# Kernel tuning notes

Hardware: AMD Instinct MI355X
Metric: run time of the kernel (lower is better)

## Reference

```python
import jax, jax.numpy as jnp
import numpy as np

ALPHA = 1.702
LIMIT = 7.0
TOP_K = 2


def setup_inputs() -> dict:
    key = jax.random.key(0)
    ks = jax.random.split(key, 5)
    B, S, H, M, E = 2, 512, 1024, 4096, 16
    glorot = jax.nn.initializers.glorot_uniform()
    return {
        "hidden_states": jax.random.normal(ks[0], (B, S, H), dtype=jnp.float32),
        "router_w": glorot(ks[1], (H, E), jnp.float32),
        "router_b": jnp.zeros((E,), jnp.float32),
        "gate_up_proj": glorot(ks[2], (E, H, 2 * M), jnp.float32),
        "gate_up_proj_bias": jnp.zeros((E, 2 * M), jnp.float32),
        "down_proj": glorot(ks[3], (E, M, H), jnp.float32),
        "down_proj_bias": jnp.zeros((E, H), jnp.float32),
    }


def _moe_forward(x, router_w, router_b, gate_up_proj, gate_up_proj_bias,
                 down_proj, down_proj_bias):
    B, S, H = x.shape
    E = router_w.shape[1]
    xt = x.reshape(-1, H)  # [T, H]
    T = xt.shape[0]

    # --- Router: top-k logits -> softmax over selected -> dense [T, E] scores ---
    logits = xt @ router_w + router_b                       # [T, E]
    top_vals, top_idx = jax.lax.top_k(logits, TOP_K)        # [T, K]
    top_w = jax.nn.softmax(top_vals, axis=-1)               # [T, K]
    router_scores = jnp.zeros((T, E), dtype=top_w.dtype).at[
        jnp.arange(T)[:, None], top_idx].add(top_w)         # [T, E]

    # --- Dense all-expert GLU-FFN (GPT-OSS dense MoE trick) ---
    gate_up = jnp.einsum('th,ehm->etm', xt, gate_up_proj)   # [E, T, 2M]
    gate_up = gate_up + gate_up_proj_bias[:, None, :]
    gate = gate_up[..., ::2]                                # interleaved split
    up = gate_up[..., 1::2]
    gate = jnp.clip(gate, -1e9, LIMIT)
    up = jnp.clip(up, -LIMIT, LIMIT)
    glu = gate * jax.nn.sigmoid(gate * ALPHA)
    gated = (up + 1.0) * glu                                # [E, T, M]
    out = jnp.einsum('etm,emh->eth', gated, down_proj)
    out = out + down_proj_bias[:, None, :]                  # [E, T, H]

    # --- Weighted combine over experts ---
    final = jnp.einsum('eth,te->th', out, router_scores)    # [T, H]
    return final.reshape(B, S, H), router_scores


def reference(hidden_states, router_w, router_b, gate_up_proj,
              gate_up_proj_bias, down_proj, down_proj_bias):
    return _moe_forward(hidden_states, router_w, router_b, gate_up_proj,
                        gate_up_proj_bias, down_proj, down_proj_bias)
```

## Files before the change

### kernel.cpp

```cpp
#include <hip/hip_runtime.h>
#include <hip/hip_bf16.h>
#include <cstdint>
#include <cstddef>

typedef unsigned short u16;
typedef __bf16 v8bf __attribute__((ext_vector_type(8)));
typedef float v4f __attribute__((ext_vector_type(4)));

#define T_TOK 1024
#define H_DIM 1024
#define E_NUM 16
#define M_DIM 4096
#define GU_DIM 8192
#define ALPHA 1.702f
#define LIMIT 7.0f
#define LDSTR 40
#define KSPL 4

#define WS_COUNTS   0
#define WS_OFFSETS  256
#define WS_TOKE     512
#define WS_TOKP     (WS_TOKE + 8192)
#define WS_TOKW     (WS_TOKP + 8192)
#define WS_TOKG     (WS_TOKW + 8192)
#define WS_SLOTTOK  (WS_TOKG + 8192)
#define WS_XG       65536
#define WS_GATED    (WS_XG + 2048*1024*2)
#define WS_OUT      (WS_GATED + (size_t)2048*4096*2)

static __device__ __forceinline__ u16 f2bf(float f) {
    union { __hip_bfloat16 b; u16 u; } cv;
    cv.b = __float2bfloat16(f);
    return cv.u;
}

__global__ __launch_bounds__(64) void k_zero(int* counts) {
    if (threadIdx.x < E_NUM) counts[threadIdx.x] = 0;
}

__global__ __launch_bounds__(64) void k_router(
    const float* __restrict__ x, const float* __restrict__ rw, const float* __restrict__ rb,
    float* __restrict__ scores, int* __restrict__ counts,
    int* __restrict__ tok_e, int* __restrict__ tok_p, float* __restrict__ tok_w)
{
    const int t = blockIdx.x;
    const int lane = threadIdx.x;
    float part[E_NUM];
#pragma unroll
    for (int e = 0; e < E_NUM; ++e) part[e] = 0.f;
    const float* xrow = x + (size_t)t * H_DIM;
    for (int h = lane; h < H_DIM; h += 64) {
        float xv = xrow[h];
        const float* wrow = rw + (size_t)h * E_NUM;
#pragma unroll
        for (int e = 0; e < E_NUM; ++e) part[e] = fmaf(xv, wrow[e], part[e]);
    }
    __shared__ float red[64][E_NUM];
    __shared__ float logits[E_NUM];
    __shared__ int se[2];
    __shared__ float sw[2];
#pragma unroll
    for (int e = 0; e < E_NUM; ++e) red[lane][e] = part[e];
    __syncthreads();
    if (lane < E_NUM) {
        float s = rb[lane];
        for (int l = 0; l < 64; ++l) s += red[l][lane];
        logits[lane] = s;
    }
    __syncthreads();
    if (lane == 0) {
        int i0 = 0; float v0 = logits[0];
        for (int e = 1; e < E_NUM; ++e) { float v = logits[e]; if (v > v0) { v0 = v; i0 = e; } }
        int i1 = -1; float v1 = -3.4e38f;
        for (int e = 0; e < E_NUM; ++e) {
            if (e == i0) continue;
            float v = logits[e];
            if (v > v1) { v1 = v; i1 = e; }
        }
        float ex = expf(v1 - v0);
        float w0 = 1.f / (1.f + ex);
        float w1 = ex / (1.f + ex);
        int p0 = atomicAdd(&counts[i0], 1);
        int p1 = atomicAdd(&counts[i1], 1);
        tok_e[2*t]   = i0; tok_p[2*t]   = p0; tok_w[2*t]   = w0;
        tok_e[2*t+1] = i1; tok_p[2*t+1] = p1; tok_w[2*t+1] = w1;
        se[0] = i0; se[1] = i1; sw[0] = w0; sw[1] = w1;
    }
    __syncthreads();
    if (lane < E_NUM) {
        float v = 0.f;
        if (lane == se[0]) v = sw[0];
        else if (lane == se[1]) v = sw[1];
        scores[(size_t)t * E_NUM + lane] = v;
    }
}

__global__ __launch_bounds__(64) void k_offsets(const int* __restrict__ counts, int* __restrict__ offsets) {
    if (threadIdx.x == 0) {
        int acc = 0;
        for (int e = 0; e < E_NUM; ++e) { offsets[e] = acc; acc += counts[e]; }
        offsets[E_NUM] = acc;
    }
}

__global__ __launch_bounds__(256) void k_build(
    const int* __restrict__ tok_e, const int* __restrict__ tok_p, const int* __restrict__ offsets,
    int* __restrict__ tok_g, int* __restrict__ slot_tok)
{
    int i = blockIdx.x * blockDim.x + threadIdx.x;
    if (i >= 2 * T_TOK) return;
    int e = tok_e[i], p = tok_p[i];
    int g = offsets[e] + p;
    tok_g[i] = g;
    slot_tok[g] = i >> 1;
}

__global__ __launch_bounds__(256) void k_gather(
    const float* __restrict__ x, const int* __restrict__ slot_tok, u16* __restrict__ xg)
{
    const int g = blockIdx.x;
    const int t = slot_tok[g];
    const float4* src = (const float4*)(x + (size_t)t * H_DIM);
    float4 v = src[threadIdx.x];
    ushort4 o;
    o.x = f2bf(v.x); o.y = f2bf(v.y); o.z = f2bf(v.z); o.w = f2bf(v.w);
    *(ushort4*)&xg[(size_t)g * H_DIM + threadIdx.x * 4] = o;
}

__global__ __launch_bounds__(512) void k_gateup(
    const u16* __restrict__ xg, const float* __restrict__ W, const float* __restrict__ bias,
    const int* __restrict__ counts, const int* __restrict__ offsets,
    u16* __restrict__ gated)
{
    const int e = blockIdx.z;
    const int cnt = counts[e];
    const int row0 = blockIdx.y * 256;
    if (row0 >= cnt) return;
    const int m0 = blockIdx.x * 64;
    const int off = offsets[e];
    __shared__ u16 As[256 * LDSTR];
    __shared__ u16 Bs[128 * LDSTR];
    const int tid = threadIdx.x;
    const int lane = tid & 63;
    const int w = tid >> 6;
    const bool active = (row0 + w * 32) < cnt;

    const int ar0 = tid >> 2, aseg = tid & 3;
    const int ar1 = ar0 + 128;
    int gr0 = row0 + ar0; if (gr0 >= cnt) gr0 = cnt - 1;
    int gr1 = row0 + ar1; if (gr1 >= cnt) gr1 = cnt - 1;
    const u16* aP0 = xg + (size_t)(off + gr0) * H_DIM + aseg * 8;
    const u16* aP1 = xg + (size_t)(off + gr1) * H_DIM + aseg * 8;

    const int bn   = tid & 127;
    const int bk0  = (tid >> 7) * 8;
    const int bcol = (bn >> 1) + (bn & 1) * 64;
    const float* bP = W + (size_t)e * H_DIM * GU_DIM + (size_t)bk0 * GU_DIM + 2 * m0 + bn;

    uint4 ra0, ra1;
    float rbA[8], rbB[8];
    v4f acc0[8], acc1[8];
    v4f zz = {0.f, 0.f, 0.f, 0.f};
#pragma unroll
    for (int f = 0; f < 8; ++f) { acc0[f] = zz; acc1[f] = zz; }

    const u16* aF = &As[(w * 32 + (lane & 15)) * LDSTR + (lane >> 4) * 8];
    const u16* bF = &Bs[(lane & 15) * LDSTR + (lane >> 4) * 8];

#define GU_LOADA(K0)                                                      \
    ra0 = *(const uint4*)(aP0 + (K0));                                    \
    ra1 = *(const uint4*)(aP1 + (K0));

#define GU_LOADB(K0, dst)                                                 \
    _Pragma("unroll")                                                     \
    for (int i = 0; i < 8; ++i) dst[i] = bP[(size_t)((K0) + i) * GU_DIM];

#define GU_STORE(rbX)                                                     \
    *(uint4*)&As[ar0 * LDSTR + aseg * 8] = ra0;                           \
    *(uint4*)&As[ar1 * LDSTR + aseg * 8] = ra1;                           \
    {                                                                     \
        uint4 p0;                                                         \
        p0.x = f2bf(rbX[0]) | ((unsigned)f2bf(rbX[1]) << 16);             \
        p0.y = f2bf(rbX[2]) | ((unsigned)f2bf(rbX[3]) << 16);             \
        p0.z = f2bf(rbX[4]) | ((unsigned)f2bf(rbX[5]) << 16);             \
        p0.w = f2bf(rbX[6]) | ((unsigned)f2bf(rbX[7]) << 16);             \
        *(uint4*)&Bs[bcol * LDSTR + bk0] = p0;                            \
    }

#define GU_MFMA                                                           \
    if (active) {                                                         \
        v8bf a0 = *(const v8bf*)aF;                                       \
        v8bf a1 = *(const v8bf*)(aF + 16 * LDSTR);                        \
        _Pragma("unroll")                                                 \
        for (int f = 0; f < 8; ++f) {                                     \
            v8bf b = *(const v8bf*)(bF + f * 16 * LDSTR);                 \
            acc0[f] = __builtin_amdgcn_mfma_f32_16x16x32_bf16(a0, b, acc0[f], 0, 0, 0); \
            acc1[f] = __builtin_amdgcn_mfma_f32_16x16x32_bf16(a1, b, acc1[f], 0, 0, 0); \
        }                                                                 \
    }

    GU_LOADA(0)
    GU_LOADB(0, rbA)
    GU_LOADB(32, rbB)
    for (int k0 = 0; k0 < H_DIM; k0 += 64) {
        GU_STORE(rbA)
        __syncthreads();
        GU_LOADA(k0 + 32)
        if (k0 + 64 < H_DIM) { GU_LOADB(k0 + 64, rbA) }
        GU_MFMA
        __syncthreads();
        GU_STORE(rbB)
        __syncthreads();
        if (k0 + 64 < H_DIM) { GU_LOADA(k0 + 64) }
        if (k0 + 96 < H_DIM) { GU_LOADB(k0 + 96, rbB) }
        GU_MFMA
        __syncthreads();
    }
#undef GU_LOADA
#undef GU_LOADB
#undef GU_STORE
#undef GU_MFMA

    if (!active) return;
    const float* bg = bias + (size_t)e * GU_DIM + 2 * m0;
#pragma unroll
    for (int i = 0; i < 2; ++i) {
#pragma unroll
        for (int r = 0; r < 4; ++r) {
            int rr = row0 + w * 32 + i * 16 + (lane >> 4) * 4 + r;
            if (rr >= cnt) continue;
            u16* orow = gated + (size_t)(off + rr) * M_DIM + m0;
#pragma unroll
            for (int f = 0; f < 4; ++f) {
                int ml = f * 16 + (lane & 15);
                float g = (i ? acc1[f][r]     : acc0[f][r])     + bg[2 * ml];
                float u = (i ? acc1[f + 4][r] : acc0[f + 4][r]) + bg[2 * ml + 1];
                g = fminf(g, LIMIT); g = fmaxf(g, -1e9f);
                u = fminf(fmaxf(u, -LIMIT), LIMIT);
                float glu = g / (1.f + expf(-ALPHA * g));
                orow[ml] = f2bf((u + 1.f) * glu);
            }
        }
    }
}

__global__ __launch_bounds__(512) void k_down(
    const u16* __restrict__ gated, const float* __restrict__ W,
    const int* __restrict__ counts, const int* __restrict__ offsets,
    float* __restrict__ outws)
{
    const int e = blockIdx.z;
    const int cnt = counts[e];
    const int row0 = blockIdx.y * 256;
    if (row0 >= cnt) return;
    const int ntile = blockIdx.x & 15;
    const int kc = blockIdx.x >> 4;
    const int c0 = ntile * 64;
    const int kbase = kc * (M_DIM / KSPL);
    const int off = offsets[e];
    __shared__ u16 As[256 * LDSTR];
    __shared__ u16 Bs[64 * LDSTR];
    const int tid = threadIdx.x;
    const int lane = tid & 63;
    const int w = tid >> 6;
    const bool active = (row0 + w * 32) < cnt;

    const int ar0 = tid >> 2, aseg = tid & 3;
    const int ar1 = ar0 + 128;
    int gr0 = row0 + ar0; if (gr0 >= cnt) gr0 = cnt - 1;
    int gr1 = row0 + ar1; if (gr1 >= cnt) gr1 = cnt - 1;
    const u16* aP0 = gated + (size_t)(off + gr0) * M_DIM + kbase + aseg * 8;
    const u16* aP1 = gated + (size_t)(off + gr1) * M_DIM + kbase + aseg * 8;

    const int bn  = tid & 63;
    const int bk0 = (tid >> 6) * 4;
    const float* bP = W + (size_t)e * M_DIM * H_DIM + (size_t)(kbase + bk0) * H_DIM + c0 + bn;

    uint4 ra0, ra1;
    float rbA[4], rbB[4];
    v4f acc0[4], acc1[4];
    v4f zz = {0.f, 0.f, 0.f, 0.f};
#pragma unroll
    for (int f = 0; f < 4; ++f) { acc0[f] = zz; acc1[f] = zz; }

    const u16* aF = &As[(w * 32 + (lane & 15)) * LDSTR + (lane >> 4) * 8];
    const u16* bF = &Bs[(lane & 15) * LDSTR + (lane >> 4) * 8];

#define DN_LOADA(K0)                                                      \
    ra0 = *(const uint4*)(aP0 + (K0));                                    \
    ra1 = *(const uint4*)(aP1 + (K0));

#define DN_LOADB(K0, dst)                                                 \
    _Pragma("unroll")                                                     \
    for (int i = 0; i < 4; ++i) dst[i] = bP[(size_t)((K0) + i) * H_DIM];

#define DN_STORE(rbX)                                                     \
    *(uint4*)&As[ar0 * LDSTR + aseg * 8] = ra0;                           \
    *(uint4*)&As[ar1 * LDSTR + aseg * 8] = ra1;                           \
    {                                                                     \
        uint2 p0;                                                         \
        p0.x = f2bf(rbX[0]) | ((unsigned)f2bf(rbX[1]) << 16);             \
        p0.y = f2bf(rbX[2]) | ((unsigned)f2bf(rbX[3]) << 16);             \
        *(uint2*)&Bs[bn * LDSTR + bk0] = p0;                              \
    }

#define DN_MFMA                                                           \
    if (active) {                                                         \
        v8bf a0 = *(const v8bf*)aF;                                       \
        v8bf a1 = *(const v8bf*)(aF + 16 * LDSTR);                        \
        _Pragma("unroll")                                                 \
        for (int f = 0; f < 4; ++f) {                                     \
            v8bf b = *(const v8bf*)(bF + f * 16 * LDSTR);                 \
            acc0[f] = __builtin_amdgcn_mfma_f32_16x16x32_bf16(a0, b, acc0[f], 0, 0, 0); \
            acc1[f] = __builtin_amdgcn_mfma_f32_16x16x32_bf16(a1, b, acc1[f], 0, 0, 0); \
        }                                                                 \
    }

    const int KC = M_DIM / KSPL;
    DN_LOADA(0)
    DN_LOADB(0, rbA)
    DN_LOADB(32, rbB)
    for (int k0 = 0; k0 < KC; k0 += 64) {
        DN_STORE(rbA)
        __syncthreads();
        DN_LOADA(k0 + 32)
        if (k0 + 64 < KC) { DN_LOADB(k0 + 64, rbA) }
        DN_MFMA
        __syncthreads();
        DN_STORE(rbB)
        __syncthreads();
        if (k0 + 64 < KC) { DN_LOADA(k0 + 64) }
        if (k0 + 96 < KC) { DN_LOADB(k0 + 96, rbB) }
        DN_MFMA
        __syncthreads();
    }
#undef DN_LOADA
#undef DN_LOADB
#undef DN_STORE
#undef DN_MFMA

    if (!active) return;
    float* outp = outws + (size_t)kc * 2048 * H_DIM;
#pragma unroll
    for (int i = 0; i < 2; ++i) {
#pragma unroll
        for (int r = 0; r < 4; ++r) {
            int rr = row0 + w * 32 + i * 16 + (lane >> 4) * 4 + r;
            if (rr >= cnt) continue;
            float* orow = outp + (size_t)(off + rr) * H_DIM + c0;
#pragma unroll
            for (int f = 0; f < 4; ++f) {
                orow[f * 16 + (lane & 15)] = (i ? acc1[f][r] : acc0[f][r]);
            }
        }
    }
}

__global__ __launch_bounds__(256) void k_final(
    const float* __restrict__ outws, const float* __restrict__ db,
    const int* __restrict__ tok_e, const int* __restrict__ tok_g, const float* __restrict__ tok_w,
    float* __restrict__ out)
{
    const int t = blockIdx.x;
    const int tid = threadIdx.x;
    const int h = tid << 2;
    const int e0 = tok_e[2*t], e1 = tok_e[2*t+1];
    const int g0 = tok_g[2*t], g1 = tok_g[2*t+1];
    const float w0 = tok_w[2*t], w1 = tok_w[2*t+1];
    float4 o0 = {0,0,0,0}, o1 = {0,0,0,0};
#pragma unroll
    for (int p = 0; p < KSPL; ++p) {
        const float* base = outws + (size_t)p * 2048 * H_DIM;
        float4 a = *(const float4*)(base + (size_t)g0 * H_DIM + h);
        float4 b = *(const float4*)(base + (size_t)g1 * H_DIM + h);
        o0.x += a.x; o0.y += a.y; o0.z += a.z; o0.w += a.w;
        o1.x += b.x; o1.y += b.y; o1.z += b.z; o1.w += b.w;
    }
    float4 b0 = *(const float4*)(db + (size_t)e0 * H_DIM + h);
    float4 b1 = *(const float4*)(db + (size_t)e1 * H_DIM + h);
    float4 r;
    r.x = w0 * (o0.x + b0.x) + w1 * (o1.x + b1.x);
    r.y = w0 * (o0.y + b0.y) + w1 * (o1.y + b1.y);
    r.z = w0 * (o0.z + b0.z) + w1 * (o1.z + b1.z);
    r.w = w0 * (o0.w + b0.w) + w1 * (o1.w + b1.w);
    *(float4*)(out + (size_t)t * H_DIM + h) = r;
}

extern "C" void kernel_launch(void* const* d_in, const int* in_sizes, int n_in,
                              void* d_out, int out_size, void* d_ws, size_t ws_size,
                              hipStream_t stream) {
    const float* x     = (const float*)d_in[0];
    const float* rw    = (const float*)d_in[1];
    const float* rb    = (const float*)d_in[2];
    const float* gup   = (const float*)d_in[3];
    const float* gup_b = (const float*)d_in[4];
    const float* dw    = (const float*)d_in[5];
    const float* db    = (const float*)d_in[6];
    float* out    = (float*)d_out;
    float* scores = out + (size_t)T_TOK * H_DIM;

    char* ws = (char*)d_ws;
    int*   counts   = (int*)(ws + WS_COUNTS);
    int*   offsets  = (int*)(ws + WS_OFFSETS);
    int*   tok_e    = (int*)(ws + WS_TOKE);
    int*   tok_p    = (int*)(ws + WS_TOKP);
    float* tok_w    = (float*)(ws + WS_TOKW);
    int*   tok_g    = (int*)(ws + WS_TOKG);
    int*   slot_tok = (int*)(ws + WS_SLOTTOK);
    u16*   xg       = (u16*)(ws + WS_XG);
    u16*   gated    = (u16*)(ws + WS_GATED);
    float* outws    = (float*)(ws + WS_OUT);

    k_zero<<<1, 64, 0, stream>>>(counts);
    k_router<<<T_TOK, 64, 0, stream>>>(x, rw, rb, scores, counts, tok_e, tok_p, tok_w);
    k_offsets<<<1, 64, 0, stream>>>(counts, offsets);
    k_build<<<(2*T_TOK + 255)/256, 256, 0, stream>>>(tok_e, tok_p, offsets, tok_g, slot_tok);
    k_gather<<<2*T_TOK, 256, 0, stream>>>(x, slot_tok, xg);
    dim3 g2(M_DIM/64, 8, E_NUM);
    k_gateup<<<g2, 512, 0, stream>>>(xg, gup, gup_b, counts, offsets, gated);
    dim3 g3(16 * KSPL, 8, E_NUM);
    k_down<<<g3, 512, 0, stream>>>(gated, dw, counts, offsets, outws);
    k_final<<<T_TOK, 256, 0, stream>>>(outws, db, tok_e, tok_g, tok_w, out);
}
```

Baseline: 270.1 us.

## Double-buffer LDS with deeper prefetch in expert GEMMs and fuse routing kernels

The gate-up and down GEMMs now use two LDS buffers with a four-deep register prefetch of weights, so each k-step needs one barrier instead of two. Weight loads become float2 vector loads with a rearranged LDS placement. launch_bounds gains a minimum of 4 blocks, and the offsets, build and gather kernels are merged into one scatter kernel that computes prefix offsets inline, saving two launches. The cost is more LDS and registers per block, and the occupancy hint can force register spills.

```diff
diff --git a/kernel.cpp b/kernel.cpp
--- a/kernel.cpp
+++ b/kernel.cpp
@@ -18,12 +18,10 @@
 #define KSPL 4
 
 #define WS_COUNTS   0
-#define WS_OFFSETS  256
 #define WS_TOKE     512
 #define WS_TOKP     (WS_TOKE + 8192)
 #define WS_TOKW     (WS_TOKP + 8192)
 #define WS_TOKG     (WS_TOKW + 8192)
-#define WS_SLOTTOK  (WS_TOKG + 8192)
 #define WS_XG       65536
 #define WS_GATED    (WS_XG + 2048*1024*2)
 #define WS_OUT      (WS_GATED + (size_t)2048*4096*2)
@@ -95,51 +93,37 @@
     }
 }
 
-__global__ __launch_bounds__(64) void k_offsets(const int* __restrict__ counts, int* __restrict__ offsets) {
-    if (threadIdx.x == 0) {
-        int acc = 0;
-        for (int e = 0; e < E_NUM; ++e) { offsets[e] = acc; acc += counts[e]; }
-        offsets[E_NUM] = acc;
-    }
-}
-
-__global__ __launch_bounds__(256) void k_build(
-    const int* __restrict__ tok_e, const int* __restrict__ tok_p, const int* __restrict__ offsets,
-    int* __restrict__ tok_g, int* __restrict__ slot_tok)
+__global__ __launch_bounds__(256) void k_scatter(
+    const float* __restrict__ x, const int* __restrict__ counts,
+    const int* __restrict__ tok_e, const int* __restrict__ tok_p,
+    int* __restrict__ tok_g, u16* __restrict__ xg)
 {
-    int i = blockIdx.x * blockDim.x + threadIdx.x;
-    if (i >= 2 * T_TOK) return;
-    int e = tok_e[i], p = tok_p[i];
-    int g = offsets[e] + p;
-    tok_g[i] = g;
-    slot_tok[g] = i >> 1;
-}
-
-__global__ __launch_bounds__(256) void k_gather(
-    const float* __restrict__ x, const int* __restrict__ slot_tok, u16* __restrict__ xg)
-{
-    const int g = blockIdx.x;
-    const int t = slot_tok[g];
-    const float4* src = (const float4*)(x + (size_t)t * H_DIM);
-    float4 v = src[threadIdx.x];
+    const int i = blockIdx.x;
+    const int e = tok_e[i], p = tok_p[i];
+    int off = 0;
+#pragma unroll
+    for (int j = 0; j < E_NUM; ++j) off += (j < e) ? counts[j] : 0;
+    const int g = off + p;
+    if (threadIdx.x == 0) tok_g[i] = g;
+    const float4 v = ((const float4*)(x + (size_t)(i >> 1) * H_DIM))[threadIdx.x];
     ushort4 o;
     o.x = f2bf(v.x); o.y = f2bf(v.y); o.z = f2bf(v.z); o.w = f2bf(v.w);
     *(ushort4*)&xg[(size_t)g * H_DIM + threadIdx.x * 4] = o;
 }
 
-__global__ __launch_bounds__(512) void k_gateup(
+__global__ __launch_bounds__(512, 4) void k_gateup(
     const u16* __restrict__ xg, const float* __restrict__ W, const float* __restrict__ bias,
-    const int* __restrict__ counts, const int* __restrict__ offsets,
-    u16* __restrict__ gated)
+    const int* __restrict__ counts, u16* __restrict__ gated)
 {
     const int e = blockIdx.z;
-    const int cnt = counts[e];
+    int cnt = 0, off = 0;
+#pragma unroll
+    for (int j = 0; j < E_NUM; ++j) { int c = counts[j]; off += (j < e) ? c : 0; if (j == e) cnt = c; }
     const int row0 = blockIdx.y * 256;
     if (row0 >= cnt) return;
     const int m0 = blockIdx.x * 64;
-    const int off = offsets[e];
-    __shared__ u16 As[256 * LDSTR];
-    __shared__ u16 Bs[128 * LDSTR];
+    __shared__ u16 As[2][256 * LDSTR];
+    __shared__ u16 Bs[2][128 * LDSTR];
     const int tid = threadIdx.x;
     const int lane = tid & 63;
     const int w = tid >> 6;
@@ -152,74 +136,95 @@
     const u16* aP0 = xg + (size_t)(off + gr0) * H_DIM + aseg * 8;
     const u16* aP1 = xg + (size_t)(off + gr1) * H_DIM + aseg * 8;
 
-    const int bn   = tid & 127;
-    const int bk0  = (tid >> 7) * 8;
-    const int bcol = (bn >> 1) + (bn & 1) * 64;
-    const float* bP = W + (size_t)e * H_DIM * GU_DIM + (size_t)bk0 * GU_DIM + 2 * m0 + bn;
+    const int bc  = tid & 63;
+    const int bkg = tid >> 6;
+    const float* bP = W + (size_t)e * H_DIM * GU_DIM + (size_t)bkg * 4 * GU_DIM + 2 * m0 + 2 * bc;
 
     uint4 ra0, ra1;
-    float rbA[8], rbB[8];
+    float rb0[8], rb1[8], rb2[8], rb3[8];
     v4f acc0[8], acc1[8];
     v4f zz = {0.f, 0.f, 0.f, 0.f};
 #pragma unroll
     for (int f = 0; f < 8; ++f) { acc0[f] = zz; acc1[f] = zz; }
 
-    const u16* aF = &As[(w * 32 + (lane & 15)) * LDSTR + (lane >> 4) * 8];
-    const u16* bF = &Bs[(lane & 15) * LDSTR + (lane >> 4) * 8];
-
-#define GU_LOADA(K0)                                                      \
-    ra0 = *(const uint4*)(aP0 + (K0));                                    \
-    ra1 = *(const uint4*)(aP1 + (K0));
-
-#define GU_LOADB(K0, dst)                                                 \
-    _Pragma("unroll")                                                     \
-    for (int i = 0; i < 8; ++i) dst[i] = bP[(size_t)((K0) + i) * GU_DIM];
-
-#define GU_STORE(rbX)                                                     \
-    *(uint4*)&As[ar0 * LDSTR + aseg * 8] = ra0;                           \
-    *(uint4*)&As[ar1 * LDSTR + aseg * 8] = ra1;                           \
+    const int aFo = (w * 32 + (lane & 15)) * LDSTR + (lane >> 4) * 8;
+    const int bFo = (lane & 15) * LDSTR + (lane >> 4) * 8;
+    const int asl0 = ar0 * LDSTR + aseg * 8;
+    const int asl1 = ar1 * LDSTR + aseg * 8;
+    const int bslg = bc * LDSTR + bkg * 4;
+    const int bslu = (bc + 64) * LDSTR + bkg * 4;
+
+#define GU_LOADA(KK)                                                      \
+    ra0 = *(const uint4*)(aP0 + (KK));                                    \
+    ra1 = *(const uint4*)(aP1 + (KK));
+
+#define GU_LOADB(KK, dst)                                                 \
     {                                                                     \
-        uint4 p0;                                                         \
-        p0.x = f2bf(rbX[0]) | ((unsigned)f2bf(rbX[1]) << 16);             \
-        p0.y = f2bf(rbX[2]) | ((unsigned)f2bf(rbX[3]) << 16);             \
-        p0.z = f2bf(rbX[4]) | ((unsigned)f2bf(rbX[5]) << 16);             \
-        p0.w = f2bf(rbX[6]) | ((unsigned)f2bf(rbX[7]) << 16);             \
-        *(uint4*)&Bs[bcol * LDSTR + bk0] = p0;                            \
-    }
-
-#define GU_MFMA                                                           \
+        const float* p_ = bP + (size_t)(KK) * GU_DIM;                     \
+        float2 t0_ = *(const float2*)(p_);                                \
+        float2 t1_ = *(const float2*)(p_ + GU_DIM);                       \
+        float2 t2_ = *(const float2*)(p_ + 2 * GU_DIM);                   \
+        float2 t3_ = *(const float2*)(p_ + 3 * GU_DIM);                   \
+        dst[0]=t0_.x; dst[1]=t0_.y; dst[2]=t1_.x; dst[3]=t1_.y;           \
+        dst[4]=t2_.x; dst[5]=t2_.y; dst[6]=t3_.x; dst[7]=t3_.y;           \
+    }
+
+#define GU_STORE(BUF, rbX)                                                \
+    *(uint4*)&As[BUF][asl0] = ra0;                                        \
+    *(uint4*)&As[BUF][asl1] = ra1;                                        \
+    {                                                                     \
+        uint2 pg_, pu_;                                                   \
+        pg_.x = f2bf(rbX[0]) | ((unsigned)f2bf(rbX[2]) << 16);            \
+        pg_.y = f2bf(rbX[4]) | ((unsigned)f2bf(rbX[6]) << 16);            \
+        pu_.x = f2bf(rbX[1]) | ((unsigned)f2bf(rbX[3]) << 16);            \
+        pu_.y = f2bf(rbX[5]) | ((unsigned)f2bf(rbX[7]) << 16);            \
+        *(uint2*)&Bs[BUF][bslg] = pg_;                                    \
+        *(uint2*)&Bs[BUF][bslu] = pu_;                                    \
+    }
+
+#define GU_MFMA(BUF)                                                      \
     if (active) {                                                         \
-        v8bf a0 = *(const v8bf*)aF;                                       \
-        v8bf a1 = *(const v8bf*)(aF + 16 * LDSTR);                        \
+        v8bf a0 = *(const v8bf*)&As[BUF][aFo];                            \
+        v8bf a1 = *(const v8bf*)&As[BUF][aFo + 16 * LDSTR];               \
         _Pragma("unroll")                                                 \
         for (int f = 0; f < 8; ++f) {                                     \
-            v8bf b = *(const v8bf*)(bF + f * 16 * LDSTR);                 \
+            v8bf b = *(const v8bf*)&Bs[BUF][bFo + f * 16 * LDSTR];        \
             acc0[f] = __builtin_amdgcn_mfma_f32_16x16x32_bf16(a0, b, acc0[f], 0, 0, 0); \
             acc1[f] = __builtin_amdgcn_mfma_f32_16x16x32_bf16(a1, b, acc1[f], 0, 0, 0); \
         }                                                                 \
     }
 
     GU_LOADA(0)
-    GU_LOADB(0, rbA)
-    GU_LOADB(32, rbB)
-    for (int k0 = 0; k0 < H_DIM; k0 += 64) {
-        GU_STORE(rbA)
-        __syncthreads();
-        GU_LOADA(k0 + 32)
-        if (k0 + 64 < H_DIM) { GU_LOADB(k0 + 64, rbA) }
-        GU_MFMA
-        __syncthreads();
-        GU_STORE(rbB)
-        __syncthreads();
-        if (k0 + 64 < H_DIM) { GU_LOADA(k0 + 64) }
-        if (k0 + 96 < H_DIM) { GU_LOADB(k0 + 96, rbB) }
-        GU_MFMA
-        __syncthreads();
-    }
+    GU_LOADB(0, rb0)
+    GU_STORE(0, rb0)
+    GU_LOADA(32)
+    GU_LOADB(32, rb1)
+    GU_LOADB(64, rb2)
+    GU_LOADB(96, rb3)
+    __syncthreads();
+
+#define GU_PH(P, RBS, RBL)                                                \
+    GU_STORE((P + 1) & 1, RBS)                                            \
+    GU_LOADA((t4 + P + 2) * 32)                                           \
+    GU_LOADB((t4 + P + 4) * 32, RBL)                                      \
+    GU_MFMA(P & 1)                                                        \
+    __syncthreads();
+
+    for (int t4 = 0; t4 < 28; t4 += 4) {
+        GU_PH(0, rb1, rb0)
+        GU_PH(1, rb2, rb1)
+        GU_PH(2, rb3, rb2)
+        GU_PH(3, rb0, rb3)
+    }
+    GU_STORE(1, rb1) GU_LOADA(960) GU_MFMA(0) __syncthreads();
+    GU_STORE(0, rb2) GU_LOADA(992) GU_MFMA(1) __syncthreads();
+    GU_STORE(1, rb3) GU_MFMA(0) __syncthreads();
+    GU_MFMA(1)
 #undef GU_LOADA
 #undef GU_LOADB
 #undef GU_STORE
 #undef GU_MFMA
+#undef GU_PH
 
     if (!active) return;
     const float* bg = bias + (size_t)e * GU_DIM + 2 * m0;
@@ -244,22 +249,22 @@
     }
 }
 
-__global__ __launch_bounds__(512) void k_down(
+__global__ __launch_bounds__(512, 4) void k_down(
     const u16* __restrict__ gated, const float* __restrict__ W,
-    const int* __restrict__ counts, const int* __restrict__ offsets,
-    float* __restrict__ outws)
+    const int* __restrict__ counts, float* __restrict__ outws)
 {
     const int e = blockIdx.z;
-    const int cnt = counts[e];
+    int cnt = 0, off = 0;
+#pragma unroll
+    for (int j = 0; j < E_NUM; ++j) { int c = counts[j]; off += (j < e) ? c : 0; if (j == e) cnt = c; }
     const int row0 = blockIdx.y * 256;
     if (row0 >= cnt) return;
     const int ntile = blockIdx.x & 15;
     const int kc = blockIdx.x >> 4;
     const int c0 = ntile * 64;
     const int kbase = kc * (M_DIM / KSPL);
-    const int off = offsets[e];
-    __shared__ u16 As[256 * LDSTR];
-    __shared__ u16 Bs[64 * LDSTR];
+    __shared__ u16 As[2][256 * LDSTR];
+    __shared__ u16 Bs[2][64 * LDSTR];
     const int tid = threadIdx.x;
     const int lane = tid & 63;
     const int w = tid >> 6;
@@ -272,72 +277,89 @@
     const u16* aP0 = gated + (size_t)(off + gr0) * M_DIM + kbase + aseg * 8;
     const u16* aP1 = gated + (size_t)(off + gr1) * M_DIM + kbase + aseg * 8;
 
-    const int bn  = tid & 63;
-    const int bk0 = (tid >> 6) * 4;
-    const float* bP = W + (size_t)e * M_DIM * H_DIM + (size_t)(kbase + bk0) * H_DIM + c0 + bn;
+    const int bc  = tid & 31;
+    const int bkg = tid >> 5;
+    const float* bP = W + (size_t)e * M_DIM * H_DIM + (size_t)(kbase + bkg * 2) * H_DIM + c0 + 2 * bc;
 
     uint4 ra0, ra1;
-    float rbA[4], rbB[4];
+    float rb0[4], rb1[4], rb2[4], rb3[4];
     v4f acc0[4], acc1[4];
     v4f zz = {0.f, 0.f, 0.f, 0.f};
 #pragma unroll
     for (int f = 0; f < 4; ++f) { acc0[f] = zz; acc1[f] = zz; }
 
-    const u16* aF = &As[(w * 32 + (lane & 15)) * LDSTR + (lane >> 4) * 8];
-    const u16* bF = &Bs[(lane & 15) * LDSTR + (lane >> 4) * 8];
-
-#define DN_LOADA(K0)                                                      \
-    ra0 = *(const uint4*)(aP0 + (K0));                                    \
-    ra1 = *(const uint4*)(aP1 + (K0));
-
-#define DN_LOADB(K0, dst)                                                 \
-    _Pragma("unroll")                                                     \
-    for (int i = 0; i < 4; ++i) dst[i] = bP[(size_t)((K0) + i) * H_DIM];
-
-#define DN_STORE(rbX)                                                     \
-    *(uint4*)&As[ar0 * LDSTR + aseg * 8] = ra0;                           \
-    *(uint4*)&As[ar1 * LDSTR + aseg * 8] = ra1;                           \
+    const int aFo = (w * 32 + (lane & 15)) * LDSTR + (lane >> 4) * 8;
+    const int bFo = (lane & 15) * LDSTR + (lane >> 4) * 8;
+    const int asl0 = ar0 * LDSTR + aseg * 8;
+    const int asl1 = ar1 * LDSTR + aseg * 8;
+    const int bsl0 = (2 * bc) * LDSTR + bkg * 2;
+    const int bsl1 = (2 * bc + 1) * LDSTR + bkg * 2;
+
+#define DN_LOADA(KK)                                                      \
+    ra0 = *(const uint4*)(aP0 + (KK));                                    \
+    ra1 = *(const uint4*)(aP1 + (KK));
+
+#define DN_LOADB(KK, dst)                                                 \
     {                                                                     \
-        uint2 p0;                                                         \
-        p0.x = f2bf(rbX[0]) | ((unsigned)f2bf(rbX[1]) << 16);             \
-        p0.y = f2bf(rbX[2]) | ((unsigned)f2bf(rbX[3]) << 16);             \
-        *(uint2*)&Bs[bn * LDSTR + bk0] = p0;                              \
-    }
-
-#define DN_MFMA                                                           \
+        const float* p_ = bP + (size_t)(KK) * H_DIM;                      \
+        float2 t0_ = *(const float2*)(p_);                                \
+        float2 t1_ = *(const float2*)(p_ + H_DIM);                        \
+        dst[0]=t0_.x; dst[1]=t0_.y; dst[2]=t1_.x; dst[3]=t1_.y;           \
+    }
+
+#define DN_STORE(BUF, rbX)                                                \
+    *(uint4*)&As[BUF][asl0] = ra0;                                        \
+    *(uint4*)&As[BUF][asl1] = ra1;                                        \
+    {                                                                     \
+        unsigned v0_ = f2bf(rbX[0]) | ((unsigned)f2bf(rbX[2]) << 16);     \
+        unsigned v1_ = f2bf(rbX[1]) | ((unsigned)f2bf(rbX[3]) << 16);     \
+        *(unsigned*)&Bs[BUF][bsl0] = v0_;                                 \
+        *(unsigned*)&Bs[BUF][bsl1] = v1_;                                 \
+    }
+
+#define DN_MFMA(BUF)                                                      \
     if (active) {                                                         \
-        v8bf a0 = *(const v8bf*)aF;                                       \
-        v8bf a1 = *(const v8bf*)(aF + 16 * LDSTR);                        \
+        v8bf a0 = *(const v8bf*)&As[BUF][aFo];                            \
+        v8bf a1 = *(const v8bf*)&As[BUF][aFo + 16 * LDSTR];               \
         _Pragma("unroll")                                                 \
         for (int f = 0; f < 4; ++f) {                                     \
-            v8bf b = *(const v8bf*)(bF + f * 16 * LDSTR);                 \
+            v8bf b = *(const v8bf*)&Bs[BUF][bFo + f * 16 * LDSTR];        \
             acc0[f] = __builtin_amdgcn_mfma_f32_16x16x32_bf16(a0, b, acc0[f], 0, 0, 0); \
             acc1[f] = __builtin_amdgcn_mfma_f32_16x16x32_bf16(a1, b, acc1[f], 0, 0, 0); \
         }                                                                 \
     }
 
-    const int KC = M_DIM / KSPL;
     DN_LOADA(0)
-    DN_LOADB(0, rbA)
-    DN_LOADB(32, rbB)
-    for (int k0 = 0; k0 < KC; k0 += 64) {
-        DN_STORE(rbA)
-        __syncthreads();
-        DN_LOADA(k0 + 32)
-        if (k0 + 64 < KC) { DN_LOADB(k0 + 64, rbA) }
-        DN_MFMA
-        __syncthreads();
-        DN_STORE(rbB)
-        __syncthreads();
-        if (k0 + 64 < KC) { DN_LOADA(k0 + 64) }
-        if (k0 + 96 < KC) { DN_LOADB(k0 + 96, rbB) }
-        DN_MFMA
-        __syncthreads();
-    }
+    DN_LOADB(0, rb0)
+    DN_STORE(0, rb0)
+    DN_LOADA(32)
+    DN_LOADB(32, rb1)
+    DN_LOADB(64, rb2)
+    DN_LOADB(96, rb3)
+    __syncthreads();
+
+#define DN_PH(P, RBS, RBL)                                                \
+    DN_STORE((P + 1) & 1, RBS)                                            \
+    DN_LOADA((t4 + P + 2) * 32)                                           \
+    DN_LOADB((t4 + P + 4) * 32, RBL)                                      \
+    DN_MFMA(P & 1)                                                        \
+    __syncthreads();
+
+    for (int t4 = 0; t4 < 28; t4 += 4) {
+        DN_PH(0, rb1, rb0)
+        DN_PH(1, rb2, rb1)
+        DN_PH(2, rb3, rb2)
+        DN_PH(3, rb0, rb3)
+    }
+    DN_STORE(1, rb1) DN_LOADA(960) DN_MFMA(0) __syncthreads();
+    DN_STORE(0, rb2) DN_LOADA(992) DN_MFMA(1) __syncthreads();
+    DN_STORE(1, rb3) DN_MFMA(0) __syncthreads();
+    DN_MFMA(1)
 #undef DN_LOADA
 #undef DN_LOADB
 #undef DN_STORE
 #undef DN_MFMA
+#undef DN_PH
 
     if (!active) return;
     float* outp = outws + (size_t)kc * 2048 * H_DIM;
@@ -401,24 +423,20 @@
 
     char* ws = (char*)d_ws;
     int*   counts   = (int*)(ws + WS_COUNTS);
-    int*   offsets  = (int*)(ws + WS_OFFSETS);
     int*   tok_e    = (int*)(ws + WS_TOKE);
     int*   tok_p    = (int*)(ws + WS_TOKP);
     float* tok_w    = (float*)(ws + WS_TOKW);
     int*   tok_g    = (int*)(ws + WS_TOKG);
-    int*   slot_tok = (int*)(ws + WS_SLOTTOK);
     u16*   xg       = (u16*)(ws + WS_XG);
     u16*   gated    = (u16*)(ws + WS_GATED);
     float* outws    = (float*)(ws + WS_OUT);
 
     k_zero<<<1, 64, 0, stream>>>(counts);
     k_router<<<T_TOK, 64, 0, stream>>>(x, rw, rb, scores, counts, tok_e, tok_p, tok_w);
-    k_offsets<<<1, 64, 0, stream>>>(counts, offsets);
-    k_build<<<(2*T_TOK + 255)/256, 256, 0, stream>>>(tok_e, tok_p, offsets, tok_g, slot_tok);
-    k_gather<<<2*T_TOK, 256, 0, stream>>>(x, slot_tok, xg);
+    k_scatter<<<2*T_TOK, 256, 0, stream>>>(x, counts, tok_e, tok_p, tok_g, xg);
     dim3 g2(M_DIM/64, 8, E_NUM);
-    k_gateup<<<g2, 512, 0, stream>>>(xg, gup, gup_b, counts, offsets, gated);
+    k_gateup<<<g2, 512, 0, stream>>>(xg, gup, gup_b, counts, gated);
     dim3 g3(16 * KSPL, 8, E_NUM);
-    k_down<<<g3, 512, 0, stream>>>(gated, dw, counts, offsets, outws);
+    k_down<<<g3, 512, 0, stream>>>(gated, dw, counts, outws);
     k_final<<<T_TOK, 256, 0, stream>>>(outws, db, tok_e, tok_g, tok_w, out);
 }
```

Measured after the change: 519.0 us. 1.92x slower.
